# Kernel optimization log

Measured on AMD Instinct MI355X. Metric: run time of the kernel, lower is better.

## Reference

```python
import jax, jax.numpy as jnp
import numpy as np

B, M, RPI = 16, 80, 256            # images, objects/image, relations/image
N, R = B * M, B * RPI
DF, REP, EMB, HID, NH, L = 12544, 1024, 256, 512, 8, 4
OBJC, RELC = 151, 51
IMW, IMH = 800.0, 600.0


def _ln(x, g, b):
    m = x.mean(-1, keepdims=True)
    v = ((x - m) ** 2).mean(-1, keepdims=True)
    return (x - m) * jax.lax.rsqrt(v + 1e-5) * g + b


def _encoder(x, qkv_w, qkv_b, out_w, out_b, f1_w, f1_b, f2_w, f2_b, ln1_s, ln1_b, ln2_s, ln2_b):
    # post-LN transformer encoder, L layers, x: [B, M, HID]
    Bb, Mm, D = x.shape
    dk = D // NH
    scale = 1.0 / jnp.sqrt(jnp.float32(dk))
    for l in range(L):
        qkv = x @ qkv_w[l].T + qkv_b[l]
        q, k, v = jnp.split(qkv, 3, axis=-1)
        hs = lambda t: t.reshape(Bb, Mm, NH, dk).transpose(0, 2, 1, 3)
        q, k, v = hs(q), hs(k), hs(v)
        att = jax.nn.softmax(jnp.einsum('bhqd,bhkd->bhqk', q, k) * scale, axis=-1)
        o = jnp.einsum('bhqk,bhkd->bhqd', att, v).transpose(0, 2, 1, 3).reshape(Bb, Mm, D)
        x = _ln(x + o @ out_w[l].T + out_b[l], ln1_s[l], ln1_b[l])
        f = jax.nn.relu(x @ f1_w[l].T + f1_b[l]) @ f2_w[l].T + f2_b[l]
        x = _ln(x + f, ln2_s[l], ln2_b[l])
    return x


def _box_info(boxes):
    wh = boxes[:, 2:] - boxes[:, :2] + 1.0
    xy = boxes[:, :2] + 0.5 * wh
    w, h = wh[:, :1], wh[:, 1:]
    x, y = xy[:, :1], xy[:, 1:]
    x1, y1, x2, y2 = boxes[:, 0:1], boxes[:, 1:2], boxes[:, 2:3], boxes[:, 3:4]
    return jnp.concatenate([w / IMW, h / IMH, x / IMW, y / IMH, x1 / IMW, y1 / IMH,
                            x2 / IMW, y2 / IMH, w * h / (IMW * IMH)], axis=-1)  # [N, 9]


def setup_inputs() -> dict:
    key = jax.random.key(0)
    ks = iter(jax.random.split(key, 80))
    nrm = lambda shape, s=0.02: jax.random.normal(next(ks), shape, jnp.float32) * s
    d = {}
    d['features'] = jax.random.normal(next(ks), (N, DF), jnp.float32)
    d['union_features'] = jax.random.normal(next(ks), (R, REP), jnp.float32)
    x1 = jax.random.uniform(next(ks), (N, 1)) * (IMW - 120.0)
    y1 = jax.random.uniform(next(ks), (N, 1)) * (IMH - 120.0)
    w = jax.random.uniform(next(ks), (N, 1)) * 100.0 + 5.0
    h = jax.random.uniform(next(ks), (N, 1)) * 100.0 + 5.0
    d['boxes'] = jnp.concatenate([x1, y1, x1 + w, y1 + h], axis=-1)
    d['logits'] = jax.random.normal(next(ks), (N, OBJC), jnp.float32)
    d['labels'] = jax.random.randint(next(ks), (N,), 0, OBJC)
    d['rel_pair_idxs'] = jax.random.randint(next(ks), (B, RPI, 2), 0, M)
    # feature extractor
    d['fe1_w'] = nrm((REP, DF)); d['fe1_b'] = jnp.zeros((REP,))
    d['fe2_w'] = nrm((REP, REP)); d['fe2_b'] = jnp.zeros((REP,))
    # embeddings
    d['emb1'] = nrm((OBJC, EMB), 1.0)
    d['emb2'] = nrm((OBJC, EMB), 1.0)
    # bbox embed 9->32->128
    d['bb1_w'] = nrm((32, 9)); d['bb1_b'] = jnp.zeros((32,))
    d['bb2_w'] = nrm((128, 32)); d['bb2_b'] = jnp.zeros((128,))
    d['lobj_w'] = nrm((HID, REP + EMB + 128)); d['lobj_b'] = jnp.zeros((HID,))
    d['ledge_w'] = nrm((HID, EMB + HID)); d['ledge_b'] = jnp.zeros((HID,))
    for p in ('o', 'e'):
        d[p + 'qkv_w'] = nrm((L, 3 * HID, HID)); d[p + 'qkv_b'] = jnp.zeros((L, 3 * HID))
        d[p + 'out_w'] = nrm((L, HID, HID)); d[p + 'out_b'] = jnp.zeros((L, HID))
        d[p + 'f1_w'] = nrm((L, HID, HID)); d[p + 'f1_b'] = jnp.zeros((L, HID))
        d[p + 'f2_w'] = nrm((L, HID, HID)); d[p + 'f2_b'] = jnp.zeros((L, HID))
        d[p + 'ln1_s'] = jnp.ones((L, HID)); d[p + 'ln1_b'] = jnp.zeros((L, HID))
        d[p + 'ln2_s'] = jnp.ones((L, HID)); d[p + 'ln2_b'] = jnp.zeros((L, HID))
    d['pcat_w'] = nrm((REP, 2 * HID)); d['pcat_b'] = jnp.zeros((REP,))
    d['fuse_w'] = nrm((REP, REP + HID)); d['fuse_b'] = jnp.zeros((REP,))
    d['cpx_w'] = nrm((RELC, 2 * REP)); d['cpx_b'] = jnp.zeros((RELC,))
    d['dpath_w'] = nrm((RELC, REP)); d['dpath_b'] = jnp.zeros((RELC,))
    return d


def reference(features, union_features, boxes, logits,
              fe1_w, fe1_b, fe2_w, fe2_b, emb1, emb2,
              bb1_w, bb1_b, bb2_w, bb2_b, lobj_w, lobj_b, ledge_w, ledge_b,
              oqkv_w, oqkv_b, oout_w, oout_b, of1_w, of1_b, of2_w, of2_b,
              oln1_s, oln1_b, oln2_s, oln2_b,
              eqkv_w, eqkv_b, eout_w, eout_b, ef1_w, ef1_b, ef2_w, ef2_b,
              eln1_s, eln1_b, eln2_s, eln2_b,
              pcat_w, pcat_b, fuse_w, fuse_b, cpx_w, cpx_b, dpath_w, dpath_b,
              labels, rel_pair_idxs):
    # FeatureExtractor
    bf = jax.nn.relu(features @ fe1_w.T + fe1_b)
    bf = jax.nn.relu(bf @ fe2_w.T + fe2_b)                        # [N, REP]
    # bbox embedding (dropout = identity in eval)
    pos = jax.nn.relu(_box_info(boxes) @ bb1_w.T + bb1_b)
    pos = jax.nn.relu(pos @ bb2_w.T + bb2_b)                      # [N, 128]
    obj_rep = jnp.concatenate([bf, emb1[labels], pos], -1) @ lobj_w.T + lobj_b  # [N, HID]
    obj_emb = _encoder(obj_rep.reshape(B, M, HID), oqkv_w, oqkv_b, oout_w, oout_b,
                       of1_w, of1_b, of2_w, of2_b, oln1_s, oln1_b, oln2_s, oln2_b)  # [B, M, HID]
    edge_in = jnp.concatenate([obj_emb.reshape(N, HID), emb2[labels]], -1) @ ledge_w.T + ledge_b
    gctx = _encoder(edge_in.reshape(B, M, HID), eqkv_w, eqkv_b, eout_w, eout_b,
                    ef1_w, ef1_b, ef2_w, ef2_b, eln1_s, eln1_b, eln2_s, eln2_b).mean(axis=1)  # [B, HID]
    # pair gather per image
    head = jax.vmap(lambda e, i: e[i])(obj_emb, rel_pair_idxs[:, :, 0])  # [B, RPI, HID]
    tail = jax.vmap(lambda e, i: e[i])(obj_emb, rel_pair_idxs[:, :, 1])
    pair = jnp.concatenate([head, tail], -1).reshape(R, 2 * HID)
    local = pair @ pcat_w.T + pcat_b                               # [R, REP]
    gexp = jnp.repeat(gctx, RPI, axis=0)                           # [R, HID]
    sem = jax.nn.relu(jnp.concatenate([local, gexp], -1) @ fuse_w.T + fuse_b)
    final = jnp.concatenate([sem, union_features], -1)             # [R, 2*REP]
    rel_logits = final @ cpx_w.T + cpx_b + local @ dpath_w.T + dpath_b  # [R, RELC]
    return rel_logits
```

## Files before the change

### kernel.cpp

```cpp
#include <hip/hip_runtime.h>
#include <hip/hip_bf16.h>
#include <cstdint>

#define DEV_INLINE __device__ __forceinline__

using u16 = unsigned short;
typedef __attribute__((ext_vector_type(8))) short bf8_t;
typedef __attribute__((ext_vector_type(4))) float f32x4;

constexpr int cB = 16, cM = 80, cRPI = 256;
constexpr int cN = cB * cM;
constexpr int cR = cB * cRPI;
constexpr int cDF = 12544, cREP = 1024, cEMB = 256, cHID = 512, cNH = 8, cL = 4;
constexpr int cRELC = 51;

DEV_INLINE u16 f2bf(float x) { return __builtin_bit_cast(u16, __float2bfloat16(x)); }
DEV_INLINE float bf2f(u16 u) { return __bfloat162float(__builtin_bit_cast(__hip_bfloat16, u)); }

DEV_INLINE float wave_max(float v) {
#pragma unroll
  for (int o = 32; o; o >>= 1) v = fmaxf(v, __shfl_xor(v, o));
  return v;
}
DEV_INLINE float wave_sum(float v) {
#pragma unroll
  for (int o = 32; o; o >>= 1) v += __shfl_xor(v, o);
  return v;
}

DEV_INLINE void gl_lds16(const u16* gp, char* lp) {
  __builtin_amdgcn_global_load_lds(
      (const __attribute__((address_space(1))) void*)gp,
      (__attribute__((address_space(3))) void*)lp, 16, 0, 0);
}

DEV_INLINE void xcd_remap(int& bx, int& by) {
  const int gx = gridDim.x;
  const int nwg = gx * gridDim.y;
  const int id = blockIdx.x + gx * blockIdx.y;
  const int q = nwg >> 3, r = nwg & 7;
  const int x = id & 7, k = id >> 3;
  const int idp = (x < r) ? x * (q + 1) + k : r * (q + 1) + (x - r) * q + k;
  bx = idp % gx;
  by = idp / gx;
}

__global__ __launch_bounds__(256) void gemm_fe1(
    const u16* __restrict__ A, const u16* __restrict__ Bw,
    float* __restrict__ outF)
{
  constexpr int lda = cDF, ldb = cDF, ldc = cREP;
  constexpr int Klen = cDF / 8;
  __shared__ u16 As[2][128 * 32];
  __shared__ u16 Bs[2][128 * 32];
  const int tid = threadIdx.x;
  const int wid = tid >> 6, lane = tid & 63;
  const int l15 = lane & 15, l4 = lane >> 4;
  const int z = blockIdx.x;
  const int tile = blockIdx.y;
  const int bm = (tile >> 3) * 128;
  const int bn = (tile & 7) * 128;
  const int wr = wid >> 1, wc = wid & 1;
  const int kbase = z * Klen;

  f32x4 acc[4][4] = {};

  auto stage = [&](int buf, int ks) {
    const int k0 = kbase + (ks << 5);
#pragma unroll
    for (int i = 0; i < 2; ++i) {
      const int cA = i * 256 + tid;
      const int row = cA >> 2, seg = cA & 3;
      const int sseg = seg ^ (row & 3);
      gl_lds16(A + (size_t)(bm + row) * lda + k0 + sseg * 8,
               (char*)As[buf] + (size_t)(cA - lane) * 16);
    }
#pragma unroll
    for (int i = 0; i < 2; ++i) {
      const int cB2 = i * 256 + tid;
      const int row = cB2 >> 2, seg = cB2 & 3;
      const int sseg = seg ^ (row & 3);
      gl_lds16(Bw + (size_t)(bn + row) * ldb + k0 + sseg * 8,
               (char*)Bs[buf] + (size_t)(cB2 - lane) * 16);
    }
  };

  const int nk = Klen >> 5;
  stage(0, 0);
  __syncthreads();

  for (int ks = 0; ks < nk; ++ks) {
    const int cur = ks & 1;
    if (ks + 1 < nk) stage(cur ^ 1, ks + 1);

    bf8_t af[4], bfr[4];
#pragma unroll
    for (int m = 0; m < 4; ++m) {
      const int r = wr * 64 + m * 16 + l15;
      const int g = l4 ^ (r & 3);
      af[m] = *(const bf8_t*)&As[cur][r * 32 + g * 8];
    }
#pragma unroll
    for (int n = 0; n < 4; ++n) {
      const int r = wc * 64 + n * 16 + l15;
      const int g = l4 ^ (r & 3);
      bfr[n] = *(const bf8_t*)&Bs[cur][r * 32 + g * 8];
    }
#pragma unroll
    for (int m = 0; m < 4; ++m)
#pragma unroll
      for (int n = 0; n < 4; ++n)
        acc[m][n] = __builtin_amdgcn_mfma_f32_16x16x32_bf16(af[m], bfr[n], acc[m][n], 0, 0, 0);
    __syncthreads();
  }

  float* po = outF + (size_t)z * cN * ldc;
#pragma unroll
  for (int m = 0; m < 4; ++m)
#pragma unroll
    for (int n = 0; n < 4; ++n) {
      const int ccol = bn + wc * 64 + n * 16 + l15;
#pragma unroll
      for (int g = 0; g < 4; ++g) {
        const int r = bm + wr * 64 + m * 16 + l4 * 4 + g;
        po[(size_t)r * ldc + ccol] = acc[m][n][g];
      }
    }
}

template <int BM, int BN, bool SPLIT>
__global__ __launch_bounds__(256) void gemm_h(
    const u16* __restrict__ A, int lda,
    const u16* __restrict__ Bw, int ldb,
    int Mr, int Nr, int Klen,
    float* __restrict__ outF, int ldc,
    u16* __restrict__ outH, int ldh,
    const float* __restrict__ bias,
    const float* __restrict__ res, int resld, int resmode,
    int relu)
{
  constexpr int MF = BM > 32 ? BM / 32 : 1, NF = BN > 32 ? BN / 32 : 1;
  constexpr int ACH = BM * 4, BCH = BN * 4;
  __shared__ u16 As[2][BM * 32];
  __shared__ u16 Bs[2][BN * 32];
  const int tid = threadIdx.x;
  const int wid = tid >> 6, lane = tid & 63;
  const int l15 = lane & 15, l4 = lane >> 4;
  int bx, by;
  xcd_remap(bx, by);
  const int bm = by * BM, bn = bx * BN;
  const int wr = wid >> 1, wc = wid & 1;
  const int kbase = SPLIT ? blockIdx.z * Klen : 0;

  f32x4 acc[MF][NF] = {};

  auto stage = [&](int buf, int ks) {
    const int k0 = kbase + (ks << 5);
#pragma unroll
    for (int i = 0; i < (ACH + 255) / 256; ++i) {
      const int cA = i * 256 + tid;
      if (ACH % 256 == 0 || cA < ACH) {
        const int row = cA >> 2, seg = cA & 3;
        const int sseg = seg ^ (row & 3);
        gl_lds16(A + (size_t)(bm + row) * lda + k0 + sseg * 8,
                 (char*)As[buf] + (size_t)(cA - lane) * 16);
      }
    }
#pragma unroll
    for (int i = 0; i < (BCH + 255) / 256; ++i) {
      const int cBp = i * 256 + ((tid + 128) & 255);
      if (BCH % 256 == 0 || cBp < BCH) {
        const int row = cBp >> 2, seg = cBp & 3;
        const int sseg = seg ^ (row & 3);
        int brow = bn + row; if (brow > Nr - 1) brow = Nr - 1;
        gl_lds16(Bw + (size_t)brow * ldb + k0 + sseg * 8,
                 (char*)Bs[buf] + (size_t)(cBp - lane) * 16);
      }
    }
  };

  const int nk = Klen >> 5;
  stage(0, 0);
  __syncthreads();

  for (int ks = 0; ks < nk; ++ks) {
    const int cur = ks & 1;
    if (ks + 1 < nk) stage(cur ^ 1, ks + 1);

    bf8_t af[MF], bfr[NF];
#pragma unroll
    for (int m = 0; m < MF; ++m) {
      const int r = wr * (BM / 2) + m * 16 + l15;
      const int g = l4 ^ (r & 3);
      af[m] = *(const bf8_t*)&As[cur][r * 32 + g * 8];
    }
#pragma unroll
    for (int n = 0; n < NF; ++n) {
      const int r = wc * (BN / 2) + n * 16 + l15;
      const int g = l4 ^ (r & 3);
      bfr[n] = *(const bf8_t*)&Bs[cur][r * 32 + g * 8];
    }
#pragma unroll
    for (int m = 0; m < MF; ++m)
#pragma unroll
      for (int n = 0; n < NF; ++n)
        acc[m][n] = __builtin_amdgcn_mfma_f32_16x16x32_bf16(af[m], bfr[n], acc[m][n], 0, 0, 0);
    __syncthreads();
  }

  if (SPLIT) {
    float* po = outF + (size_t)blockIdx.z * Mr * ldc;
#pragma unroll
    for (int m = 0; m < MF; ++m)
#pragma unroll
      for (int n = 0; n < NF; ++n) {
        const int ccol = bn + wc * (BN / 2) + n * 16 + l15;
        if (ccol >= Nr) continue;
#pragma unroll
        for (int g = 0; g < 4; ++g) {
          const int r = bm + wr * (BM / 2) + m * 16 + l4 * 4 + g;
          po[(size_t)r * ldc + ccol] = acc[m][n][g];
        }
      }
  } else {
#pragma unroll
    for (int m = 0; m < MF; ++m)
#pragma unroll
      for (int n = 0; n < NF; ++n) {
        const int ccol = bn + wc * (BN / 2) + n * 16 + l15;
        if (ccol >= Nr) continue;
        const float bv = bias ? bias[ccol] : 0.f;
#pragma unroll
        for (int g = 0; g < 4; ++g) {
          const int r = bm + wr * (BM / 2) + m * 16 + l4 * 4 + g;
          float v = acc[m][n][g] + bv;
          if (resmode == 1) v += res[(size_t)r * resld + ccol];
          else if (resmode == 2) v += res[(size_t)(r >> 8) * resld + ccol];
          if (relu) v = fmaxf(v, 0.f);
          if (outF) outF[(size_t)r * ldc + ccol] = v;
          if (outH) outH[(size_t)r * ldh + ccol] = f2bf(v);
        }
      }
  }
}

template <int BM, int BN>
static void g16(hipStream_t s, const u16* A, int lda, const u16* W, int ldb,
                int M, int N, int K, float* outF, int ldc, u16* outH, int ldh,
                const float* bias, const float* res, int resld, int resmode, int relu) {
  dim3 g((N + BN - 1) / BN, M / BM);
  gemm_h<BM, BN, false><<<g, 256, 0, s>>>(A, lda, W, ldb, M, N, K, outF, ldc, outH, ldh,
                                          bias, res, resld, resmode, relu);
}

__global__ void conv_big2(const float* __restrict__ f, const float* __restrict__ w,
                          u16* __restrict__ fh, u16* __restrict__ wh) {
  constexpr int N1 = cN * cDF / 4;
  constexpr int N2 = cREP * cDF / 4;
  for (int i = blockIdx.x * 256 + threadIdx.x; i < N1 + N2; i += gridDim.x * 256) {
    const float4 v = (i < N1) ? ((const float4*)f)[i] : ((const float4*)w)[i - N1];
    ushort4 o = {f2bf(v.x), f2bf(v.y), f2bf(v.z), f2bf(v.w)};
    if (i < N1) ((ushort4*)fh)[i] = o; else ((ushort4*)wh)[i - N1] = o;
  }
}

constexpr size_t W_FE2 = 0, W_LOBJ = W_FE2 + 1048576, W_LEDGE = W_LOBJ + 720896,
  W_OQKV = W_LEDGE + 393216, W_OOUT = W_OQKV + 3145728, W_OF1 = W_OOUT + 1048576,
  W_OF2 = W_OF1 + 1048576, W_EQKV = W_OF2 + 1048576, W_EOUT = W_EQKV + 3145728,
  W_EF1 = W_EOUT + 1048576, W_EF2 = W_EF1 + 1048576, W_PCAT = W_EF2 + 1048576,
  W_FUSE = W_PCAT + 1048576, W_WEND = W_FUSE + 1572864;

struct EncSrcs {
  const float *fe2, *lobj, *ledge, *oqkv, *oout, *of1, *of2,
              *eqkv, *eout, *ef1, *ef2, *pcat, *fuse;
};

__global__ void conv_enc(EncSrcs S, u16* __restrict__ wb) {
#define SEG(nm, OFF, PRE, LEN) \
  if (i < (PRE) + (LEN)) { \
    const float4 v = ((const float4*)S.nm)[i - (PRE)]; \
    ushort4 o = {f2bf(v.x), f2bf(v.y), f2bf(v.z), f2bf(v.w)}; \
    ((ushort4*)(wb + (OFF)))[i - (PRE)] = o; \
  } else
  for (int i = blockIdx.x * 256 + threadIdx.x; i < (int)(W_WEND / 4); i += gridDim.x * 256) {
    SEG(fe2,  W_FE2,   0,       262144)
    SEG(lobj, W_LOBJ,  262144,  180224)
    SEG(ledge,W_LEDGE, 442368,  98304)
    SEG(oqkv, W_OQKV,  540672,  786432)
    SEG(oout, W_OOUT,  1327104, 262144)
    SEG(of1,  W_OF1,   1589248, 262144)
    SEG(of2,  W_OF2,   1851392, 262144)
    SEG(eqkv, W_EQKV,  2113536, 786432)
    SEG(eout, W_EOUT,  2899968, 262144)
    SEG(ef1,  W_EF1,   3162112, 262144)
    SEG(ef2,  W_EF2,   3424256, 262144)
    SEG(pcat, W_PCAT,  3686400, 262144)
    SEG(fuse, W_FUSE,  3948544, 393216)
    { }
  }
#undef SEG
}

__global__ void conv_cat(const float* __restrict__ cpx, const float* __restrict__ dpath,
                         const float* __restrict__ cb, const float* __restrict__ db,
                         u16* __restrict__ catw, float* __restrict__ biasc) {
  constexpr int N1 = cRELC * 512;
  constexpr int N2 = cRELC * 256;
  const int i0 = blockIdx.x * 256 + threadIdx.x;
  if (blockIdx.x == 0 && threadIdx.x < cRELC) biasc[threadIdx.x] = cb[threadIdx.x] + db[threadIdx.x];
  for (int i = i0; i < N1 + N2; i += gridDim.x * 256) {
    if (i < N1) {
      const int r = i >> 9, c = i & 511;
      const float4 v = ((const float4*)cpx)[i];
      ushort4 o = {f2bf(v.x), f2bf(v.y), f2bf(v.z), f2bf(v.w)};
      ((ushort4*)catw)[r * 768 + c] = o;
    } else {
      const int j = i - N1, r = j >> 8, c = j & 255;
      const float4 v = ((const float4*)dpath)[j];
      ushort4 o = {f2bf(v.x), f2bf(v.y), f2bf(v.z), f2bf(v.w)};
      ((ushort4*)catw)[r * 768 + 512 + c] = o;
    }
  }
}

__global__ void conv2d_kernel(const float* __restrict__ src, int slda,
                              u16* __restrict__ dst, int dld, int cols) {
  const int r = blockIdx.x;
  for (int c = threadIdx.x; c < cols; c += blockDim.x)
    dst[(size_t)r * dld + c] = f2bf(src[(size_t)r * slda + c]);
}

__global__ __launch_bounds__(256) void prep_obj(
    const float* __restrict__ boxes,
    const float* __restrict__ bb1w, const float* __restrict__ bb1b,
    const float* __restrict__ bb2w, const float* __restrict__ bb2b,
    const float* __restrict__ emb1, const int* __restrict__ labels,
    u16* __restrict__ obj_in) {
  __shared__ float W1[288];
  __shared__ float W2[4096];
  __shared__ float P1[8][33];
  const int tid = threadIdx.x;
  for (int i = tid; i < 288; i += 256) W1[i] = bb1w[i];
  for (int i = tid; i < 4096; i += 256) W2[i] = bb2w[i];
  __syncthreads();
  const int r8 = tid >> 5, sub = tid & 31;
  const int row = blockIdx.x * 8 + r8;
  const float x1 = boxes[row * 4], y1 = boxes[row * 4 + 1];
  const float x2 = boxes[row * 4 + 2], y2 = boxes[row * 4 + 3];
  const float w = x2 - x1 + 1.f, h = y2 - y1 + 1.f;
  const float bi[9] = {w / 800.f, h / 600.f, (x1 + 0.5f * w) / 800.f, (y1 + 0.5f * h) / 600.f,
                       x1 / 800.f, y1 / 600.f, x2 / 800.f, y2 / 600.f, w * h / 480000.f};
  float p = bb1b[sub];
#pragma unroll
  for (int j = 0; j < 9; ++j) p += bi[j] * W1[sub * 9 + j];
  P1[r8][sub] = fmaxf(p, 0.f);
  __syncthreads();
#pragma unroll
  for (int jo = 0; jo < 4; ++jo) {
    const int o = sub + jo * 32;
    float a = bb2b[o];
#pragma unroll
    for (int j2 = 0; j2 < 32; ++j2) a += P1[r8][j2] * W2[o * 32 + j2];
    obj_in[(size_t)row * 1408 + 1280 + o] = f2bf(fmaxf(a, 0.f));
  }
  const int l = labels[row];
#pragma unroll
  for (int k = 0; k < 8; ++k)
    obj_in[(size_t)row * 1408 + 1024 + sub + k * 32] = f2bf(emb1[(size_t)l * 256 + sub + k * 32]);
}

__global__ void gather_pair(const float* __restrict__ emb2, const int* __restrict__ labels,
                            u16* __restrict__ edge_in,
                            const int* __restrict__ idx, u16* __restrict__ pair) {
  const int r = blockIdx.x;
  const int tid = threadIdx.x;
  if (r < cN) {
    const int l = labels[r];
    edge_in[(size_t)r * 768 + 512 + tid] = f2bf(emb2[(size_t)l * cEMB + tid]);
  }
  const int b = r >> 8, rr = r & 255;
  const int i0 = idx[(size_t)(b * cRPI + rr) * 2 + 0];
  const int i1 = idx[(size_t)(b * cRPI + rr) * 2 + 1];
  const u16* hsrc = edge_in + (size_t)(b * cM + i0) * 768;
  const u16* tsrc = edge_in + (size_t)(b * cM + i1) * 768;
  u16* p = pair + (size_t)r * 1024;
  for (int c = tid; c < cHID; c += blockDim.x) {
    p[c] = hsrc[c];
    p[cHID + c] = tsrc[c];
  }
}

__global__ __launch_bounds__(256) void attn_kernel(const u16* __restrict__ qkv,
                                                   u16* __restrict__ o) {
  __shared__ float Ks[80][65];
  __shared__ float Vs[80][65];
  const int bh = blockIdx.x;
  const int b = bh >> 3, h = bh & 7;
  const int tid = threadIdx.x;
  const u16* base = qkv + (size_t)(b * cM) * 1536 + h * 64;

  for (int e = tid; e < 640; e += 256) {
    const int r = e >> 3, d0 = (e & 7) * 8;
    const bf8_t kv = *(const bf8_t*)&base[(size_t)r * 1536 + 512 + d0];
    const bf8_t vv = *(const bf8_t*)&base[(size_t)r * 1536 + 1024 + d0];
#pragma unroll
    for (int j = 0; j < 8; ++j) {
      Ks[r][d0 + j] = bf2f((u16)kv[j]);
      Vs[r][d0 + j] = bf2f((u16)vv[j]);
    }
  }
  __syncthreads();

  const int wave = tid >> 6, lane = tid & 63;
  const int r0 = blockIdx.y * 16;
  for (int r = r0 + wave; r < r0 + 16; r += 4) {
    const float qd = bf2f(base[(size_t)r * 1536 + lane]);
    const int c2 = 64 + lane;
    const int c2c = (c2 < 80) ? c2 : 0;
    float s0 = 0.f, s1 = 0.f;
#pragma unroll 8
    for (int d = 0; d < 64; ++d) {
      const float qv = __shfl(qd, d);
      s0 += qv * Ks[lane][d];
      s1 += qv * Ks[c2c][d];
    }
    s0 *= 0.125f;
    s1 = (c2 < 80) ? s1 * 0.125f : -1e30f;
    const float mx = wave_max(fmaxf(s0, s1));
    const float p0 = __expf(s0 - mx);
    const float p1 = (c2 < 80) ? __expf(s1 - mx) : 0.f;
    const float ssum = wave_sum(p0 + p1);

    float od = 0.f;
#pragma unroll 8
    for (int c = 0; c < 64; ++c) od += __shfl(p0, c) * Vs[c][lane];
#pragma unroll
    for (int c = 0; c < 16; ++c) od += __shfl(p1, c) * Vs[64 + c][lane];
    od /= ssum;
    o[(size_t)(b * cM + r) * cHID + h * 64 + lane] = f2bf(od);
  }
}

__global__ __launch_bounds__(256) void ln_kernel(
    const float* __restrict__ in, float* __restrict__ outF,
    u16* __restrict__ outH, int ldh,
    const float* __restrict__ g, const float* __restrict__ bta) {
  const int row = blockIdx.x * 4 + (threadIdx.x >> 6);
  const int lane = threadIdx.x & 63;
  const float* x = in + (size_t)row * cHID;
  float v[8];
  float s = 0.f;
#pragma unroll
  for (int i = 0; i < 8; ++i) { v[i] = x[lane + i * 64]; s += v[i]; }
  s = wave_sum(s);
  const float mean = s * (1.f / 512.f);
  float vs = 0.f;
#pragma unroll
  for (int i = 0; i < 8; ++i) { const float d = v[i] - mean; vs += d * d; }
  vs = wave_sum(vs);
  const float inv = rsqrtf(vs * (1.f / 512.f) + 1e-5f);
#pragma unroll
  for (int i = 0; i < 8; ++i) {
    const int c = lane + i * 64;
    const float y = (v[i] - mean) * inv * g[c] + bta[c];
    outF[(size_t)row * cHID + c] = y;
    outH[(size_t)row * ldh + c] = f2bf(y);
  }
}

__global__ void mean_kernel(const float* __restrict__ x, u16* __restrict__ gctx_h) {
  const int b = blockIdx.x;
  const int c = threadIdx.x;
  float s = 0.f;
  for (int m = 0; m < cM; ++m) s += x[(size_t)(b * cM + m) * cHID + c];
  gctx_h[(size_t)b * cHID + c] = f2bf(s * (1.f / 80.f));
}

__global__ void reduce8_kernel(const float* __restrict__ p, const float* __restrict__ bias,
                               u16* __restrict__ outH) {
  const int idx = blockIdx.x * 256 + threadIdx.x;
  constexpr int total = cN * cREP;
  if (idx >= total) return;
  float v = bias[idx & 1023];
#pragma unroll
  for (int z = 0; z < 8; ++z) v += p[(size_t)z * total + idx];
  outH[idx] = f2bf(fmaxf(v, 0.f));
}

__global__ void freduce_kernel(const float* __restrict__ p, const float* __restrict__ biasc,
                               float* __restrict__ out) {
  const int idx = blockIdx.x * 256 + threadIdx.x;
  if (idx >= cR * cRELC) return;
  const int r = idx / cRELC, c = idx - r * cRELC;
  float v = biasc[c];
#pragma unroll
  for (int z = 0; z < 4; ++z) v += p[(size_t)z * cR * 64 + (size_t)r * 64 + c];
  out[idx] = v;
}

static void run_encoder(hipStream_t s, float* x, u16* xh, u16* qkvh, u16* attn_h,
                        float* res1, u16* f_h,
                        const u16* qkvw, const float* qkvb,
                        const u16* outw, const float* outb,
                        const u16* f1w, const float* f1b,
                        const u16* f2w, const float* f2b,
                        const float* ln1s, const float* ln1b,
                        const float* ln2s, const float* ln2b,
                        u16* last_bf, int last_ld) {
  for (int l = 0; l < cL; ++l) {
    g16<32, 32>(s, xh, 512, qkvw + (size_t)l * 1536 * 512, 512, cN, 1536, 512,
                nullptr, 0, qkvh, 1536, qkvb + l * 1536, nullptr, 0, 0, 0);
    attn_kernel<<<dim3(cB * cNH, 5), 256, 0, s>>>(qkvh, attn_h);
    g16<32, 32>(s, attn_h, 512, outw + (size_t)l * 512 * 512, 512, cN, 512, 512,
                res1, 512, nullptr, 0, outb + l * 512, x, 512, 1, 0);
    ln_kernel<<<cN / 4, 256, 0, s>>>(res1, x, xh, 512, ln1s + l * 512, ln1b + l * 512);
    g16<32, 32>(s, xh, 512, f1w + (size_t)l * 512 * 512, 512, cN, 512, 512,
                nullptr, 0, f_h, 512, f1b + l * 512, nullptr, 0, 0, 1);
    g16<32, 32>(s, f_h, 512, f2w + (size_t)l * 512 * 512, 512, cN, 512, 512,
                res1, 512, nullptr, 0, f2b + l * 512, x, 512, 1, 0);
    const bool last = (l == cL - 1);
    ln_kernel<<<cN / 4, 256, 0, s>>>(res1, x, last ? last_bf : xh, last ? last_ld : 512,
                                     ln2s + l * 512, ln2b + l * 512);
  }
}

constexpr size_t OFF_FEAT  = 0;
constexpr size_t OFF_FE1W  = 32112640;
constexpr size_t OFF_PART  = 57802752;
constexpr size_t P_END     = 99745792;
constexpr size_t OFF_PAIR  = 0;
constexpr size_t OFF_FINAL = 8388608;
constexpr size_t OFF_OBJIN = 33554432;
constexpr size_t OFF_QKVH  = 37158912;
constexpr size_t OFF_X     = 41091072;
constexpr size_t OFF_XH    = 43712512;
constexpr size_t OFF_ATTN  = 45023232;
constexpr size_t OFF_RES   = 46333952;
constexpr size_t OFF_FH    = 48955392;
constexpr size_t OFF_EDGE  = 50266112;

extern "C" void kernel_launch(void* const* d_in, const int* in_sizes, int n_in,
                              void* d_out, int out_size, void* d_ws, size_t ws_size,
                              hipStream_t stream) {
  (void)in_sizes; (void)n_in; (void)out_size; (void)ws_size;

  const float* features = (const float*)d_in[0];
  const float* unionf   = (const float*)d_in[1];
  const float* boxes    = (const float*)d_in[2];
  const int*   labels   = (const int*)d_in[4];
  const int*   relidx   = (const int*)d_in[5];
  const float* fe1_w = (const float*)d_in[6];
  const float* fe1_b = (const float*)d_in[7];
  const float* fe2_w = (const float*)d_in[8];
  const float* fe2_b = (const float*)d_in[9];
  const float* emb1  = (const float*)d_in[10];
  const float* emb2  = (const float*)d_in[11];
  const float* bb1_w = (const float*)d_in[12];
  const float* bb1_b = (const float*)d_in[13];
  const float* bb2_w = (const float*)d_in[14];
  const float* bb2_b = (const float*)d_in[15];
  const float* lobj_w = (const float*)d_in[16];
  const float* lobj_b = (const float*)d_in[17];
  const float* ledge_w = (const float*)d_in[18];
  const float* ledge_b = (const float*)d_in[19];
  const float* oqkv_w = (const float*)d_in[20];
  const float* oqkv_b = (const float*)d_in[21];
  const float* oout_w = (const float*)d_in[22];
  const float* oout_b = (const float*)d_in[23];
  const float* of1_w = (const float*)d_in[24];
  const float* of1_b = (const float*)d_in[25];
  const float* of2_w = (const float*)d_in[26];
  const float* of2_b = (const float*)d_in[27];
  const float* oln1_s = (const float*)d_in[28];
  const float* oln1_b = (const float*)d_in[29];
  const float* oln2_s = (const float*)d_in[30];
  const float* oln2_b = (const float*)d_in[31];
  const float* eqkv_w = (const float*)d_in[32];
  const float* eqkv_b = (const float*)d_in[33];
  const float* eout_w = (const float*)d_in[34];
  const float* eout_b = (const float*)d_in[35];
  const float* ef1_w = (const float*)d_in[36];
  const float* ef1_b = (const float*)d_in[37];
  const float* ef2_w = (const float*)d_in[38];
  const float* ef2_b = (const float*)d_in[39];
  const float* eln1_s = (const float*)d_in[40];
  const float* eln1_b = (const float*)d_in[41];
  const float* eln2_s = (const float*)d_in[42];
  const float* eln2_b = (const float*)d_in[43];
  const float* pcat_w = (const float*)d_in[44];
  const float* pcat_b = (const float*)d_in[45];
  const float* fuse_w = (const float*)d_in[46];
  const float* fuse_b = (const float*)d_in[47];
  const float* cpx_w  = (const float*)d_in[48];
  const float* cpx_b  = (const float*)d_in[49];
  const float* dpath_w = (const float*)d_in[50];
  const float* dpath_b = (const float*)d_in[51];

  char* wsb = (char*)d_ws;
  u16* feat_h  = (u16*)(wsb + OFF_FEAT);
  u16* fe1w_h  = (u16*)(wsb + OFF_FE1W);
  float* part  = (float*)(wsb + OFF_PART);
  u16* pair    = (u16*)(wsb + OFF_PAIR);
  u16* finalb  = (u16*)(wsb + OFF_FINAL);
  u16* obj_in  = (u16*)(wsb + OFF_OBJIN);
  u16* qkvh    = (u16*)(wsb + OFF_QKVH);
  float* x     = (float*)(wsb + OFF_X);
  u16* xh      = (u16*)(wsb + OFF_XH);
  u16* attn_h  = (u16*)(wsb + OFF_ATTN);
  float* res1  = (float*)(wsb + OFF_RES);
  u16* f_h     = (u16*)(wsb + OFF_FH);
  u16* edge_in = (u16*)(wsb + OFF_EDGE);

  size_t off = P_END;
  auto alloc = [&](size_t bytes) { char* p = wsb + off; off = (off + bytes + 255) & ~(size_t)255; return p; };
  u16* wblock   = (u16*)alloc(W_WEND * 2);
  u16* catw     = (u16*)alloc(313344);
  float* biasc  = (float*)alloc(256);
  u16* bf0h     = (u16*)alloc(2621440);
  u16* gctx_h   = (u16*)alloc(65536);
  float* gcproj = (float*)alloc(262144);
  float* fpart  = (float*)alloc(4194304);

  const u16* fe2w_h   = wblock + W_FE2;
  const u16* lobjw_h  = wblock + W_LOBJ;
  const u16* ledgew_h = wblock + W_LEDGE;
  const u16* pcatw_h  = wblock + W_PCAT;
  const u16* fusew_h  = wblock + W_FUSE;

  conv_big2<<<2048, 256, 0, stream>>>(features, fe1_w, feat_h, fe1w_h);
  EncSrcs es = {fe2_w, lobj_w, ledge_w, oqkv_w, oout_w, of1_w, of2_w,
                eqkv_w, eout_w, ef1_w, ef2_w, pcat_w, fuse_w};
  conv_enc<<<2048, 256, 0, stream>>>(es, wblock);
  conv_cat<<<160, 256, 0, stream>>>(cpx_w, dpath_w, cpx_b, dpath_b, catw, biasc);

  gemm_fe1<<<dim3(8, 80), 256, 0, stream>>>(feat_h, fe1w_h, part);
  reduce8_kernel<<<(cN * cREP + 255) / 256, 256, 0, stream>>>(part, fe1_b, bf0h);

  prep_obj<<<cN / 8, 256, 0, stream>>>(boxes, bb1_w, bb1_b, bb2_w, bb2_b, emb1, labels, obj_in);

  g16<32, 32>(stream, bf0h, 1024, fe2w_h, 1024, cN, cREP, cREP,
              nullptr, 0, obj_in, 1408, fe2_b, nullptr, 0, 0, 1);

  g16<32, 32>(stream, obj_in, 1408, lobjw_h, 1408, cN, cHID, 1408,
              x, 512, xh, 512, lobj_b, nullptr, 0, 0, 0);

  run_encoder(stream, x, xh, qkvh, attn_h, res1, f_h,
              wblock + W_OQKV, oqkv_b, wblock + W_OOUT, oout_b,
              wblock + W_OF1, of1_b, wblock + W_OF2, of2_b,
              oln1_s, oln1_b, oln2_s, oln2_b, edge_in, 768);

  gather_pair<<<cR, 256, 0, stream>>>(emb2, labels, edge_in, relidx, pair);

  g16<32, 32>(stream, edge_in, 768, ledgew_h, 768, cN, cHID, 768,
              x, 512, xh, 512, ledge_b, nullptr, 0, 0, 0);
  run_encoder(stream, x, xh, qkvh, attn_h, res1, f_h,
              wblock + W_EQKV, eqkv_b, wblock + W_EOUT, eout_b,
              wblock + W_EF1, ef1_b, wblock + W_EF2, ef2_b,
              eln1_s, eln1_b, eln2_s, eln2_b, xh, 512);
  mean_kernel<<<cB, cHID, 0, stream>>>(x, gctx_h);

  g16<32, 64>(stream, gctx_h, 512, fusew_h + 1024, 1536, 64, cREP, 512,
              gcproj, 1024, nullptr, 0, fuse_b, nullptr, 0, 0, 0);

  conv2d_kernel<<<cR, 256, 0, stream>>>(unionf, 1024, finalb + 1024, 3072, 1024);
  g16<128, 64>(stream, pair, 1024, pcatw_h, 1024, cR, cREP, 1024,
               nullptr, 0, finalb + 2048, 3072, pcat_b, nullptr, 0, 0, 0);
  g16<128, 64>(stream, finalb + 2048, 3072, fusew_h, 1536, cR, cREP, 1024,
               nullptr, 0, finalb, 3072, nullptr, gcproj, 1024, 2, 1);

  gemm_h<64, 64, true><<<dim3(1, 64, 4), 256, 0, stream>>>(
      finalb, 3072, catw, 3072, cR, cRELC, 3072 / 4, fpart, 64,
      nullptr, 0, nullptr, nullptr, 0, 0, 0);
  freduce_kernel<<<(cR * cRELC + 255) / 256, 256, 0, stream>>>(fpart, biasc, (float*)d_out);
}
```

Baseline: 872.0 us.

## Fuse fp32-to-bf16 conversion into the big split-K feature GEMM loads

Removes the separate conversion pass over the features and fe1 weight matrices. The split-K GEMM now reads fp32 directly into registers, converts to bf16 and writes LDS after the MFMA block, giving register-staged prefetch. This avoids writing and re-reading about 57 MB of bf16 intermediates. The cost is twice the global bytes per tile load inside the GEMM and higher register pressure, and the tile loads no longer use direct-to-LDS copies.

```diff
diff --git a/kernel.cpp b/kernel.cpp
--- a/kernel.cpp
+++ b/kernel.cpp
@@ -16,6 +16,15 @@
 
 DEV_INLINE u16 f2bf(float x) { return __builtin_bit_cast(u16, __float2bfloat16(x)); }
 DEV_INLINE float bf2f(u16 u) { return __bfloat162float(__builtin_bit_cast(__hip_bfloat16, u)); }
+
+DEV_INLINE bf8_t cvt8(float4 a, float4 b) {
+  bf8_t r;
+  r[0] = (short)f2bf(a.x); r[1] = (short)f2bf(a.y);
+  r[2] = (short)f2bf(a.z); r[3] = (short)f2bf(a.w);
+  r[4] = (short)f2bf(b.x); r[5] = (short)f2bf(b.y);
+  r[6] = (short)f2bf(b.z); r[7] = (short)f2bf(b.w);
+  return r;
+}
 
 DEV_INLINE float wave_max(float v) {
 #pragma unroll
@@ -46,7 +55,7 @@
 }
 
 __global__ __launch_bounds__(256) void gemm_fe1(
-    const u16* __restrict__ A, const u16* __restrict__ Bw,
+    const float* __restrict__ A, const float* __restrict__ Bw,
     float* __restrict__ outF)
 {
   constexpr int lda = cDF, ldb = cDF, ldc = cREP;
@@ -63,35 +72,45 @@
   const int wr = wid >> 1, wc = wid & 1;
   const int kbase = z * Klen;
 
+  const int c0 = tid,        r0g = c0 >> 2, g0 = c0 & 3, s0 = g0 ^ (r0g & 3);
+  const int c1 = 256 + tid,  r1g = c1 >> 2, g1 = c1 & 3, s1 = g1 ^ (r1g & 3);
+  const float* a0p = A + (size_t)(bm + r0g) * lda + kbase + s0 * 8;
+  const float* a1p = A + (size_t)(bm + r1g) * lda + kbase + s1 * 8;
+  const float* b0p = Bw + (size_t)(bn + r0g) * ldb + kbase + s0 * 8;
+  const float* b1p = Bw + (size_t)(bn + r1g) * ldb + kbase + s1 * 8;
+  u16* a0d = &As[0][r0g * 32 + g0 * 8];
+  u16* a1d = &As[0][r1g * 32 + g1 * 8];
+  u16* b0d = &Bs[0][r0g * 32 + g0 * 8];
+  u16* b1d = &Bs[0][r1g * 32 + g1 * 8];
+  constexpr int BUFO = 128 * 32;
+
   f32x4 acc[4][4] = {};
 
-  auto stage = [&](int buf, int ks) {
-    const int k0 = kbase + (ks << 5);
-#pragma unroll
-    for (int i = 0; i < 2; ++i) {
-      const int cA = i * 256 + tid;
-      const int row = cA >> 2, seg = cA & 3;
-      const int sseg = seg ^ (row & 3);
-      gl_lds16(A + (size_t)(bm + row) * lda + k0 + sseg * 8,
-               (char*)As[buf] + (size_t)(cA - lane) * 16);
-    }
-#pragma unroll
-    for (int i = 0; i < 2; ++i) {
-      const int cB2 = i * 256 + tid;
-      const int row = cB2 >> 2, seg = cB2 & 3;
-      const int sseg = seg ^ (row & 3);
-      gl_lds16(Bw + (size_t)(bn + row) * ldb + k0 + sseg * 8,
-               (char*)Bs[buf] + (size_t)(cB2 - lane) * 16);
-    }
+  float4 va0, va1, va2, va3, vb0, vb1, vb2, vb3;
+  auto loadRegs = [&](int ks) {
+    const int k = ks << 5;
+    const float4* p;
+    p = (const float4*)(a0p + k); va0 = p[0]; va1 = p[1];
+    p = (const float4*)(a1p + k); va2 = p[0]; va3 = p[1];
+    p = (const float4*)(b0p + k); vb0 = p[0]; vb1 = p[1];
+    p = (const float4*)(b1p + k); vb2 = p[0]; vb3 = p[1];
   };
+  auto writeLds = [&](int buf) {
+    const int o = buf * BUFO;
+    *(bf8_t*)(a0d + o) = cvt8(va0, va1);
+    *(bf8_t*)(a1d + o) = cvt8(va2, va3);
+    *(bf8_t*)(b0d + o) = cvt8(vb0, vb1);
+    *(bf8_t*)(b1d + o) = cvt8(vb2, vb3);
+  };
 
   const int nk = Klen >> 5;
-  stage(0, 0);
+  loadRegs(0);
+  writeLds(0);
   __syncthreads();
 
   for (int ks = 0; ks < nk; ++ks) {
     const int cur = ks & 1;
-    if (ks + 1 < nk) stage(cur ^ 1, ks + 1);
+    if (ks + 1 < nk) loadRegs(ks + 1);
 
     bf8_t af[4], bfr[4];
 #pragma unroll
@@ -111,6 +130,8 @@
 #pragma unroll
       for (int n = 0; n < 4; ++n)
         acc[m][n] = __builtin_amdgcn_mfma_f32_16x16x32_bf16(af[m], bfr[n], acc[m][n], 0, 0, 0);
+
+    if (ks + 1 < nk) writeLds(cur ^ 1);
     __syncthreads();
   }
 
@@ -253,17 +274,6 @@
                                           bias, res, resld, resmode, relu);
 }
 
-__global__ void conv_big2(const float* __restrict__ f, const float* __restrict__ w,
-                          u16* __restrict__ fh, u16* __restrict__ wh) {
-  constexpr int N1 = cN * cDF / 4;
-  constexpr int N2 = cREP * cDF / 4;
-  for (int i = blockIdx.x * 256 + threadIdx.x; i < N1 + N2; i += gridDim.x * 256) {
-    const float4 v = (i < N1) ? ((const float4*)f)[i] : ((const float4*)w)[i - N1];
-    ushort4 o = {f2bf(v.x), f2bf(v.y), f2bf(v.z), f2bf(v.w)};
-    if (i < N1) ((ushort4*)fh)[i] = o; else ((ushort4*)wh)[i - N1] = o;
-  }
-}
-
 constexpr size_t W_FE2 = 0, W_LOBJ = W_FE2 + 1048576, W_LEDGE = W_LOBJ + 720896,
   W_OQKV = W_LEDGE + 393216, W_OOUT = W_OQKV + 3145728, W_OF1 = W_OOUT + 1048576,
   W_OF2 = W_OF1 + 1048576, W_EQKV = W_OF2 + 1048576, W_EOUT = W_EQKV + 3145728,
@@ -524,8 +534,6 @@
   }
 }
 
-constexpr size_t OFF_FEAT  = 0;
-constexpr size_t OFF_FE1W  = 32112640;
 constexpr size_t OFF_PART  = 57802752;
 constexpr size_t P_END     = 99745792;
 constexpr size_t OFF_PAIR  = 0;
@@ -597,8 +605,6 @@
   const float* dpath_b = (const float*)d_in[51];
 
   char* wsb = (char*)d_ws;
-  u16* feat_h  = (u16*)(wsb + OFF_FEAT);
-  u16* fe1w_h  = (u16*)(wsb + OFF_FE1W);
   float* part  = (float*)(wsb + OFF_PART);
   u16* pair    = (u16*)(wsb + OFF_PAIR);
   u16* finalb  = (u16*)(wsb + OFF_FINAL);
@@ -627,14 +633,13 @@
   const u16* pcatw_h  = wblock + W_PCAT;
   const u16* fusew_h  = wblock + W_FUSE;
 
-  conv_big2<<<2048, 256, 0, stream>>>(features, fe1_w, feat_h, fe1w_h);
+  gemm_fe1<<<dim3(8, 80), 256, 0, stream>>>(features, fe1_w, part);
+  reduce8_kernel<<<(cN * cREP + 255) / 256, 256, 0, stream>>>(part, fe1_b, bf0h);
+
   EncSrcs es = {fe2_w, lobj_w, ledge_w, oqkv_w, oout_w, of1_w, of2_w,
                 eqkv_w, eout_w, ef1_w, ef2_w, pcat_w, fuse_w};
   conv_enc<<<2048, 256, 0, stream>>>(es, wblock);
   conv_cat<<<160, 256, 0, stream>>>(cpx_w, dpath_w, cpx_b, dpath_b, catw, biasc);
-
-  gemm_fe1<<<dim3(8, 80), 256, 0, stream>>>(feat_h, fe1w_h, part);
-  reduce8_kernel<<<(cN * cREP + 255) / 256, 256, 0, stream>>>(part, fe1_b, bf0h);
 
   prep_obj<<<cN / 8, 256, 0, stream>>>(boxes, bb1_w, bb1_b, bb2_w, bb2_b, emb1, labels, obj_in);
 
```

Result: no change. 885.9 us (+1.6%).
